# Kernel optimization log

Hardware: AMD Instinct MI355X
Metric: run time of the kernel (lower is better)

## Reference

```python
import jax, jax.numpy as jnp
import numpy as np

B, D = 64, 512          # batch, in_dims
P, PS, S = 128, 3, 64   # num_patches, patch_size, scene_size


def setup_inputs() -> dict:
    key = jax.random.key(0)
    k0, k1, k2, k3 = jax.random.split(key, 4)
    z = jax.random.normal(k0, (B, D), jnp.float32)
    Wm = jax.random.normal(k1, (P * PS * PS, D), jnp.float32) * 0.02
    bm = jnp.zeros((P * PS * PS,), jnp.float32)
    Wt = jax.random.normal(k2, (6 * P, D), jnp.float32) * 0.01
    # module initializes transform bias to [scale,0,0,0,scale,0] per patch (scale=2)
    bt = jnp.tile(jnp.array([2.0, 0.0, 0.0, 0.0, 2.0, 0.0], jnp.float32), P)
    noise = jax.random.normal(k3, (PS, PS), jnp.float32)
    return {"z": z, "Wm": Wm, "bm": bm, "Wt": Wt, "bt": bt, "noise": noise}


def _affine_grid(theta, size):
    # theta: (N,2,3). Matches torch affine_grid(align_corners=False).
    c = (jnp.arange(size, dtype=theta.dtype) + 0.5) / size * 2.0 - 1.0
    xg, yg = jnp.meshgrid(c, c)  # xg[h,w]=c[w], yg[h,w]=c[h]
    base = jnp.stack([xg, yg, jnp.ones_like(xg)], axis=-1)  # (S,S,3)
    return jnp.einsum('nij,hwj->nhwi', theta, base)  # (N,S,S,2), [...,0]=x, [...,1]=y


def _grid_sample_bilinear_zeros(img, grid):
    # img: (N,Hi,Wi), grid: (N,Ho,Wo,2). torch grid_sample bilinear, zeros padding,
    # align_corners=False.
    N, Hi, Wi = img.shape
    ix = ((grid[..., 0] + 1.0) * Wi - 1.0) * 0.5
    iy = ((grid[..., 1] + 1.0) * Hi - 1.0) * 0.5
    ix0 = jnp.floor(ix)
    iy0 = jnp.floor(iy)
    wx1 = ix - ix0
    wy1 = iy - iy0
    wx0 = 1.0 - wx1
    wy0 = 1.0 - wy1
    b = jnp.arange(N)[:, None, None]

    def gather(xf, yf):
        xi = xf.astype(jnp.int32)
        yi = yf.astype(jnp.int32)
        valid = (xi >= 0) & (xi < Wi) & (yi >= 0) & (yi < Hi)
        xc = jnp.clip(xi, 0, Wi - 1)
        yc = jnp.clip(yi, 0, Hi - 1)
        return jnp.where(valid, img[b, yc, xc], 0.0)

    v00 = gather(ix0, iy0)
    v01 = gather(ix0 + 1.0, iy0)
    v10 = gather(ix0, iy0 + 1.0)
    v11 = gather(ix0 + 1.0, iy0 + 1.0)
    return (wy0 * (wx0 * v00 + wx1 * v01) + wy1 * (wx0 * v10 + wx1 * v11))


def reference(z, Wm, bm, Wt, bt, noise):
    Bz = z.shape[0]
    # refine_patches=True path: masks = 1 - sigmoid(Linear(z))
    masks = 1.0 - jax.nn.sigmoid(z @ Wm.T + bm)
    masks = masks.reshape(Bz, P, PS, PS) * noise  # patch_noise multiply
    theta = (z @ Wt.T + bt).reshape(Bz, P, 2, 3)
    imgs = masks.reshape(Bz * P, PS, PS)
    th = theta.reshape(Bz * P, 2, 3)
    grid = _affine_grid(th, S)                      # (B*P, S, S, 2)
    out = _grid_sample_bilinear_zeros(imgs, grid)   # (B*P, S, S)
    return out.reshape(Bz, P, S, S)
```

## Files before the change

### kernel.cpp

```cpp
#include <hip/hip_runtime.h>
#include <math.h>

#define BATCH 64
#define DIM 512
#define NPATCH 128
#define SSZ 64
#define NMASK 1152
#define NTHETA 768
#define NROWS 1920

__global__ __launch_bounds__(256) void k1_gemm(
    const float* __restrict__ z, const float* __restrict__ Wm,
    const float* __restrict__ bm, const float* __restrict__ Wt,
    const float* __restrict__ bt, const float* __restrict__ noise,
    float* __restrict__ tmp) {
  __shared__ float zs[64][65];
  __shared__ float ws[16][64];

  const int t = threadIdx.x;
  const int rowBase = blockIdx.x * 16;
  const int b = t & 63;
  const int rgrp = t >> 6;

  float acc0 = 0.f, acc1 = 0.f, acc2 = 0.f, acc3 = 0.f;

  const int zb = t >> 2, zseg = t & 3;
  const int wrow = t >> 4, wseg = t & 15;
  const int j_w = rowBase + wrow;
  const float* wsrc = (j_w < NMASK) ? (Wm + (size_t)j_w * DIM)
                                    : (Wt + (size_t)(j_w - NMASK) * DIM);

  for (int kc = 0; kc < DIM; kc += 64) {
    __syncthreads();
    {
      const float4* zsrc4 = (const float4*)(z + (size_t)zb * DIM + kc + zseg * 16);
      float* zd = &zs[zb][zseg * 16];
#pragma unroll
      for (int u = 0; u < 4; ++u) {
        float4 a = zsrc4[u];
        zd[u * 4 + 0] = a.x; zd[u * 4 + 1] = a.y;
        zd[u * 4 + 2] = a.z; zd[u * 4 + 3] = a.w;
      }
    }
    {
      float4 wv = *(const float4*)(wsrc + kc + wseg * 4);
      *(float4*)&ws[wrow][wseg * 4] = wv;
    }
    __syncthreads();
#pragma unroll 8
    for (int k = 0; k < 64; ++k) {
      float zv = zs[b][k];
      acc0 = fmaf(zv, ws[rgrp * 4 + 0][k], acc0);
      acc1 = fmaf(zv, ws[rgrp * 4 + 1][k], acc1);
      acc2 = fmaf(zv, ws[rgrp * 4 + 2][k], acc2);
      acc3 = fmaf(zv, ws[rgrp * 4 + 3][k], acc3);
    }
  }

  float accs[4] = {acc0, acc1, acc2, acc3};
#pragma unroll
  for (int rr = 0; rr < 4; ++rr) {
    int j = rowBase + rgrp * 4 + rr;
    float v = accs[rr];
    if (j < NMASK) {
      v = 1.0f / (1.0f + expf(v + bm[j]));
      v *= noise[j % 9];
    } else {
      v += bt[j - NMASK];
    }
    tmp[(size_t)j * 64 + b] = v;
  }
}

__global__ __launch_bounds__(256) void k2_sample(
    const float* __restrict__ tmp, float* __restrict__ out) {
  __shared__ float sm[15];

  const int t = threadIdx.x;
  const int bp = blockIdx.x;
  const int b = bp >> 7;
  const int p = bp & 127;

  if (t < 9) {
    sm[t] = tmp[(size_t)(p * 9 + t) * 64 + b];
  } else if (t < 15) {
    sm[t] = tmp[(size_t)(NMASK + p * 6 + (t - 9)) * 64 + b];
  }
  __syncthreads();

  const float m00 = sm[0], m01 = sm[1], m02 = sm[2];
  const float m10 = sm[3], m11 = sm[4], m12 = sm[5];
  const float m20 = sm[6], m21 = sm[7], m22 = sm[8];
  const float th0 = sm[9], th1 = sm[10], th2 = sm[11];
  const float th3 = sm[12], th4 = sm[13], th5 = sm[14];

  const int w4 = (t & 15) << 2;
  const int hb = t >> 4;
  const float cx0 = (w4 + 0.5f) * (1.0f / 32.0f) - 1.0f;
  const float cy0 = (hb + 0.5f) * (1.0f / 32.0f) - 1.0f;
  const float dix = th0 * (1.5f / 32.0f);
  const float diy = th3 * (1.5f / 32.0f);
  const float Bx = 1.5f * th1, By = 1.5f * th4;
  const float Px = fmaf(1.5f, fmaf(th0, cx0, th2), 1.0f);
  const float Py = fmaf(1.5f, fmaf(th3, cx0, th5), 1.0f);

  float* op = out + ((size_t)bp << 12) + hb * 64 + w4;

#pragma unroll
  for (int i = 0; i < 4; ++i) {
    const float cy = cy0 + 0.5f * i;
    float ix = fmaf(Bx, cy, Px);
    float iy = fmaf(By, cy, Py);
    float4 r;
    float* rp = &r.x;
#pragma unroll
    for (int j = 0; j < 4; ++j) {
      const float wx0 = fmaxf(1.0f - fabsf(ix), 0.0f);
      const float wx1 = fmaxf(1.0f - fabsf(ix - 1.0f), 0.0f);
      const float wx2 = fmaxf(1.0f - fabsf(ix - 2.0f), 0.0f);
      const float wy0 = fmaxf(1.0f - fabsf(iy), 0.0f);
      const float wy1 = fmaxf(1.0f - fabsf(iy - 1.0f), 0.0f);
      const float wy2 = fmaxf(1.0f - fabsf(iy - 2.0f), 0.0f);
      const float s0 = fmaf(m02, wx2, fmaf(m01, wx1, m00 * wx0));
      const float s1 = fmaf(m12, wx2, fmaf(m11, wx1, m10 * wx0));
      const float s2 = fmaf(m22, wx2, fmaf(m21, wx1, m20 * wx0));
      rp[j] = fmaf(wy2, s2, fmaf(wy1, s1, wy0 * s0));
      ix += dix;
      iy += diy;
    }
    *(float4*)(op + i * 16 * 64) = r;
  }
}

extern "C" void kernel_launch(void* const* d_in, const int* in_sizes, int n_in,
                              void* d_out, int out_size, void* d_ws, size_t ws_size,
                              hipStream_t stream) {
  const float* z     = (const float*)d_in[0];
  const float* Wm    = (const float*)d_in[1];
  const float* bm    = (const float*)d_in[2];
  const float* Wt    = (const float*)d_in[3];
  const float* bt    = (const float*)d_in[4];
  const float* noise = (const float*)d_in[5];
  float* out = (float*)d_out;
  float* tmp = (float*)d_ws;

  hipLaunchKernelGGL(k1_gemm, dim3(NROWS / 16), dim3(256), 0, stream,
                     z, Wm, bm, Wt, bt, noise, tmp);
  hipLaunchKernelGGL(k2_sample, dim3(BATCH * NPATCH), dim3(256), 0, stream,
                     tmp, out);
}
```

Before: 162.5 us.

## Fuse linear projection into sampling kernel, computing per-patch dot products in-block

Removes the separate GEMM kernel and its workspace round-trip. Each sampling block now computes its own 15 dot products (9 mask rows, 6 theta rows) of length 512 against its batch row, with 16 threads per row and a shuffle reduction. This saves one launch and the intermediate buffer. In exchange, weight rows are re-read once per batch element (64 times), which is mostly served from cache, and the block has extra latency before it starts the 16 KB output write.

New measurement: 161.2 us. About the same (-0.8%).

```diff
diff --git a/kernel.cpp b/kernel.cpp
--- a/kernel.cpp
+++ b/kernel.cpp
@@ -5,86 +5,49 @@
 #define DIM 512
 #define NPATCH 128
 #define SSZ 64
-#define NMASK 1152
-#define NTHETA 768
-#define NROWS 1920
 
-__global__ __launch_bounds__(256) void k1_gemm(
+__global__ __launch_bounds__(256) void k_fused(
     const float* __restrict__ z, const float* __restrict__ Wm,
     const float* __restrict__ bm, const float* __restrict__ Wt,
     const float* __restrict__ bt, const float* __restrict__ noise,
-    float* __restrict__ tmp) {
-  __shared__ float zs[64][65];
-  __shared__ float ws[16][64];
-
-  const int t = threadIdx.x;
-  const int rowBase = blockIdx.x * 16;
-  const int b = t & 63;
-  const int rgrp = t >> 6;
-
-  float acc0 = 0.f, acc1 = 0.f, acc2 = 0.f, acc3 = 0.f;
-
-  const int zb = t >> 2, zseg = t & 3;
-  const int wrow = t >> 4, wseg = t & 15;
-  const int j_w = rowBase + wrow;
-  const float* wsrc = (j_w < NMASK) ? (Wm + (size_t)j_w * DIM)
-                                    : (Wt + (size_t)(j_w - NMASK) * DIM);
-
-  for (int kc = 0; kc < DIM; kc += 64) {
-    __syncthreads();
-    {
-      const float4* zsrc4 = (const float4*)(z + (size_t)zb * DIM + kc + zseg * 16);
-      float* zd = &zs[zb][zseg * 16];
-#pragma unroll
-      for (int u = 0; u < 4; ++u) {
-        float4 a = zsrc4[u];
-        zd[u * 4 + 0] = a.x; zd[u * 4 + 1] = a.y;
-        zd[u * 4 + 2] = a.z; zd[u * 4 + 3] = a.w;
-      }
-    }
-    {
-      float4 wv = *(const float4*)(wsrc + kc + wseg * 4);
-      *(float4*)&ws[wrow][wseg * 4] = wv;
-    }
-    __syncthreads();
-#pragma unroll 8
-    for (int k = 0; k < 64; ++k) {
-      float zv = zs[b][k];
-      acc0 = fmaf(zv, ws[rgrp * 4 + 0][k], acc0);
-      acc1 = fmaf(zv, ws[rgrp * 4 + 1][k], acc1);
-      acc2 = fmaf(zv, ws[rgrp * 4 + 2][k], acc2);
-      acc3 = fmaf(zv, ws[rgrp * 4 + 3][k], acc3);
-    }
-  }
-
-  float accs[4] = {acc0, acc1, acc2, acc3};
-#pragma unroll
-  for (int rr = 0; rr < 4; ++rr) {
-    int j = rowBase + rgrp * 4 + rr;
-    float v = accs[rr];
-    if (j < NMASK) {
-      v = 1.0f / (1.0f + expf(v + bm[j]));
-      v *= noise[j % 9];
-    } else {
-      v += bt[j - NMASK];
-    }
-    tmp[(size_t)j * 64 + b] = v;
-  }
-}
-
-__global__ __launch_bounds__(256) void k2_sample(
-    const float* __restrict__ tmp, float* __restrict__ out) {
-  __shared__ float sm[15];
+    float* __restrict__ out) {
+  __shared__ float sm[16];
 
   const int t = threadIdx.x;
   const int bp = blockIdx.x;
   const int b = bp >> 7;
   const int p = bp & 127;
 
-  if (t < 9) {
-    sm[t] = tmp[(size_t)(p * 9 + t) * 64 + b];
-  } else if (t < 15) {
-    sm[t] = tmp[(size_t)(NMASK + p * 6 + (t - 9)) * 64 + b];
+  const int r = t >> 4;
+  const int c = t & 15;
+  float acc = 0.0f;
+  if (r < 15) {
+    const float* __restrict__ wrow =
+        (r < 9) ? (Wm + (size_t)(p * 9 + r) * DIM)
+                : (Wt + (size_t)(p * 6 + (r - 9)) * DIM);
+    const float* __restrict__ zrow = z + (size_t)b * DIM;
+#pragma unroll
+    for (int i = 0; i < 8; ++i) {
+      const float4 wv = *(const float4*)(wrow + i * 64 + c * 4);
+      const float4 zv = *(const float4*)(zrow + i * 64 + c * 4);
+      acc = fmaf(wv.x, zv.x, acc);
+      acc = fmaf(wv.y, zv.y, acc);
+      acc = fmaf(wv.z, zv.z, acc);
+      acc = fmaf(wv.w, zv.w, acc);
+    }
+  }
+  acc += __shfl_xor(acc, 1);
+  acc += __shfl_xor(acc, 2);
+  acc += __shfl_xor(acc, 4);
+  acc += __shfl_xor(acc, 8);
+  if (c == 0 && r < 15) {
+    float v = acc;
+    if (r < 9) {
+      v = (1.0f / (1.0f + expf(v + bm[p * 9 + r]))) * noise[r];
+    } else {
+      v += bt[p * 6 + (r - 9)];
+    }
+    sm[r] = v;
   }
   __syncthreads();
 
@@ -111,8 +74,8 @@
     const float cy = cy0 + 0.5f * i;
     float ix = fmaf(Bx, cy, Px);
     float iy = fmaf(By, cy, Py);
-    float4 r;
-    float* rp = &r.x;
+    float4 rv;
+    float* rp = &rv.x;
 #pragma unroll
     for (int j = 0; j < 4; ++j) {
       const float wx0 = fmaxf(1.0f - fabsf(ix), 0.0f);
@@ -128,7 +91,7 @@
       ix += dix;
       iy += diy;
     }
-    *(float4*)(op + i * 16 * 64) = r;
+    *(float4*)(op + i * 16 * 64) = rv;
   }
 }
 
@@ -142,10 +105,7 @@
   const float* bt    = (const float*)d_in[4];
   const float* noise = (const float*)d_in[5];
   float* out = (float*)d_out;
-  float* tmp = (float*)d_ws;
 
-  hipLaunchKernelGGL(k1_gemm, dim3(NROWS / 16), dim3(256), 0, stream,
-                     z, Wm, bm, Wt, bt, noise, tmp);
-  hipLaunchKernelGGL(k2_sample, dim3(BATCH * NPATCH), dim3(256), 0, stream,
-                     tmp, out);
+  hipLaunchKernelGGL(k_fused, dim3(BATCH * NPATCH), dim3(256), 0, stream,
+                     z, Wm, bm, Wt, bt, noise, out);
 }
```
